# Kernel tuning notes

Measured on AMD Instinct MI355X. Metric: run time of the kernel, lower is better.

The kernel has to match this reference:

```python
import jax, jax.numpy as jnp
import numpy as np

B, NPG, D = 512, 200, 256  # graphs, nodes-per-graph, d_model
N = B * NPG
STEP = 4


def setup_inputs() -> dict:
    key = jax.random.key(0)
    ks = jax.random.split(key, 7)
    def xav(k, shape):
        fan_in, fan_out = shape[1], shape[0]
        std = float(np.sqrt(2.0 / (fan_in + fan_out)))
        return jax.random.normal(k, shape, jnp.float32) * std
    return {
        "node": jax.random.normal(ks[0], (N, D), jnp.float32),
        "node_num": jnp.full((B,), NPG, dtype=jnp.int32),
        "W_ih": xav(ks[1], (4 * D, 2 * D)),  # lstm weight_ih_l0
        "W_hh": xav(ks[2], (4 * D, D)),      # lstm weight_hh_l0
        "b_ih": jnp.zeros((4 * D,), jnp.float32),
        "b_hh": jnp.zeros((4 * D,), jnp.float32),
        "Wo": xav(ks[3], (D, 2 * D)),        # W_o.weight
        "bo": jnp.zeros((D,), jnp.float32),  # W_o.bias
    }


def reference(node, node_num, W_ih, W_hh, b_ih, b_hh, Wo, bo):
    n_total, d = node.shape
    bsz = node_num.shape[0]
    batch_idx = jnp.repeat(jnp.arange(bsz), node_num, total_repeat_length=n_total)
    h = jnp.zeros((bsz, d), node.dtype)
    c = jnp.zeros((bsz, d), node.dtype)
    q_star = jnp.zeros((bsz, 2 * d), node.dtype)
    for _ in range(STEP):
        # single-step LSTM (torch gate order: i, f, g, o)
        gates = q_star @ W_ih.T + h @ W_hh.T + b_ih + b_hh
        i, f, g, o = jnp.split(gates, 4, axis=-1)
        c = jax.nn.sigmoid(f) * c + jax.nn.sigmoid(i) * jnp.tanh(g)
        h = jax.nn.sigmoid(o) * jnp.tanh(c)
        q = h  # [B, d]
        # segmented softmax attention over nodes
        e = jnp.sum(node * q[batch_idx], axis=-1)  # [N]
        emax = jax.ops.segment_max(e, batch_idx, num_segments=bsz)
        e = jnp.exp(e - emax[batch_idx])
        denom = jax.ops.segment_sum(e, batch_idx, num_segments=bsz)
        a = e / (denom[batch_idx] + 1e-6)
        r = jax.ops.segment_sum(a[:, None] * node, batch_idx, num_segments=bsz)
        q_star = jnp.concatenate([q, r], axis=-1)
    return q_star @ Wo.T + bo
```

## Files before the change

kernel.cpp:

```cpp
#include <hip/hip_runtime.h>
#include <math.h>

#define DCH 256
#define BSZ 512
#define NPG 200
#define G4  1024
#define K2  512
#define KSD 4

typedef __attribute__((ext_vector_type(8))) short short8v;
typedef __attribute__((ext_vector_type(4))) float f32x4;

__device__ __forceinline__ float sigf(float x) { return 1.0f / (1.0f + __expf(-x)); }

__device__ __forceinline__ unsigned pack2bf(float a, float b) {
    unsigned ua = __float_as_uint(a), ub = __float_as_uint(b);
    ua = (ua + 0x7FFFu + ((ua >> 16) & 1u)) >> 16;
    ub = (ub + 0x7FFFu + ((ub >> 16) & 1u)) & 0xFFFF0000u;
    return ua | ub;
}
__device__ __forceinline__ float lo_bf(unsigned u) { return __uint_as_float(u << 16); }
__device__ __forceinline__ float hi_bf(unsigned u) { return __uint_as_float(u & 0xFFFF0000u); }

__global__ __launch_bounds__(256) void prep_kernel(
    const float* __restrict__ W_ih, const float* __restrict__ W_hh,
    const float* __restrict__ Wo,
    uint4* __restrict__ wcat, uint4* __restrict__ wobf)
{
    int idx = blockIdx.x * 256 + threadIdx.x;
    if (idx < 65536) {
        const int n = idx >> 6, k = (idx & 63) * 8;
        float v[8];
        *(float4*)(v)     = *(const float4*)(W_ih + (size_t)n * K2 + k);
        *(float4*)(v + 4) = *(const float4*)(W_ih + (size_t)n * K2 + k + 4);
        if (k < DCH) {
            float h[8];
            *(float4*)(h)     = *(const float4*)(W_hh + (size_t)n * DCH + k);
            *(float4*)(h + 4) = *(const float4*)(W_hh + (size_t)n * DCH + k + 4);
            #pragma unroll
            for (int i = 0; i < 8; ++i) v[i] += h[i];
        }
        uint4 u;
        u.x = pack2bf(v[0], v[1]); u.y = pack2bf(v[2], v[3]);
        u.z = pack2bf(v[4], v[5]); u.w = pack2bf(v[6], v[7]);
        wcat[idx] = u;
    } else {
        idx -= 65536;
        const int n = idx >> 6, k = (idx & 63) * 8;
        float v[8];
        *(float4*)(v)     = *(const float4*)(Wo + (size_t)n * K2 + k);
        *(float4*)(v + 4) = *(const float4*)(Wo + (size_t)n * K2 + k + 4);
        uint4 u;
        u.x = pack2bf(v[0], v[1]); u.y = pack2bf(v[2], v[3]);
        u.z = pack2bf(v[4], v[5]); u.w = pack2bf(v[6], v[7]);
        wobf[idx] = u;
    }
}

__global__ __launch_bounds__(256) void gemm_gates_mfma(
    const unsigned short* __restrict__ hrbf,
    const unsigned short* __restrict__ wcat,
    float* __restrict__ gpart, int Kper)
{
    const int wid  = threadIdx.x >> 6;
    const int lane = threadIdx.x & 63;
    const int bm = blockIdx.y * 64;
    const int bn = blockIdx.x * 128 + wid * 32;
    const int kbase = blockIdx.z * Kper;
    const int rsel = lane & 15, kgrp = lane >> 4;

    f32x4 acc00 = {}, acc01 = {}, acc10 = {}, acc11 = {},
          acc20 = {}, acc21 = {}, acc30 = {}, acc31 = {};

    for (int k0 = 0; k0 < Kper; k0 += 32) {
        const int kk = kbase + k0 + kgrp * 8;
        short8v a0 = *(const short8v*)(hrbf + (size_t)(bm +  0 + rsel) * K2 + kk);
        short8v a1 = *(const short8v*)(hrbf + (size_t)(bm + 16 + rsel) * K2 + kk);
        short8v a2 = *(const short8v*)(hrbf + (size_t)(bm + 32 + rsel) * K2 + kk);
        short8v a3 = *(const short8v*)(hrbf + (size_t)(bm + 48 + rsel) * K2 + kk);
        short8v b0 = *(const short8v*)(wcat + (size_t)(bn +  0 + rsel) * K2 + kk);
        short8v b1 = *(const short8v*)(wcat + (size_t)(bn + 16 + rsel) * K2 + kk);
        acc00 = __builtin_amdgcn_mfma_f32_16x16x32_bf16(a0, b0, acc00, 0, 0, 0);
        acc01 = __builtin_amdgcn_mfma_f32_16x16x32_bf16(a0, b1, acc01, 0, 0, 0);
        acc10 = __builtin_amdgcn_mfma_f32_16x16x32_bf16(a1, b0, acc10, 0, 0, 0);
        acc11 = __builtin_amdgcn_mfma_f32_16x16x32_bf16(a1, b1, acc11, 0, 0, 0);
        acc20 = __builtin_amdgcn_mfma_f32_16x16x32_bf16(a2, b0, acc20, 0, 0, 0);
        acc21 = __builtin_amdgcn_mfma_f32_16x16x32_bf16(a2, b1, acc21, 0, 0, 0);
        acc30 = __builtin_amdgcn_mfma_f32_16x16x32_bf16(a3, b0, acc30, 0, 0, 0);
        acc31 = __builtin_amdgcn_mfma_f32_16x16x32_bf16(a3, b1, acc31, 0, 0, 0);
    }

    float* Cp = gpart + (size_t)blockIdx.z * BSZ * G4;
    const int crow = kgrp * 4, ccol = rsel;
    const f32x4* accs[4][2] = { {&acc00, &acc01}, {&acc10, &acc11},
                                {&acc20, &acc21}, {&acc30, &acc31} };
    #pragma unroll
    for (int mi = 0; mi < 4; ++mi)
        #pragma unroll
        for (int ni = 0; ni < 2; ++ni)
            #pragma unroll
            for (int r = 0; r < 4; ++r)
                Cp[(size_t)(bm + mi * 16 + crow + r) * G4 + bn + ni * 16 + ccol] =
                    (*accs[mi][ni])[r];
}

template<int FIRST, int LAST>
__global__ __launch_bounds__(256) void lstm_attn_kernel(
    const float* __restrict__ gpart,
    const float* __restrict__ b_ih, const float* __restrict__ b_hh,
    const float* __restrict__ node, uint4* __restrict__ nbf,
    const int* __restrict__ node_num,
    float* __restrict__ cbuf, unsigned* __restrict__ hrbf,
    const uint4* __restrict__ wobf, const float* __restrict__ bo,
    float* __restrict__ outp)
{
    __shared__ __align__(16) float smem[4640];
    float* qs = smem;
    float (*red_r)[DCH] = (float (*)[DCH])(smem + 512);
    float* red_m = smem + 4608;
    float* red_s = smem + 4624;

    const int b = blockIdx.x;
    const int t = threadIdx.x;

    float gv[4];
    #pragma unroll
    for (int q = 0; q < 4; ++q) {
        const int idx = q * DCH + t;
        float v = b_ih[idx] + b_hh[idx];
        if (!FIRST) {
            #pragma unroll
            for (int z = 0; z < KSD; ++z)
                v += gpart[(size_t)z * BSZ * G4 + (size_t)b * G4 + idx];
        }
        gv[q] = v;
    }
    const float c_old = FIRST ? 0.0f : cbuf[b * DCH + t];
    const float cn = sigf(gv[1]) * c_old + sigf(gv[0]) * tanhf(gv[2]);
    const float hn = sigf(gv[3]) * tanhf(cn);
    if (!LAST) cbuf[b * DCH + t] = cn;
    qs[t] = hn;
    __syncthreads();

    const int w = t >> 6, l = t & 63;
    const int p = l & 15;
    const int g = w * 4 + (l >> 4);
    const int cnt = node_num[b];
    const float* nb = node + (size_t)b * NPG * DCH;
    uint4* nbf_b = nbf + (size_t)b * NPG * 32;

    float4 qv[4];
    #pragma unroll
    for (int j = 0; j < 2; ++j) {
        qv[j*2+0] = *(const float4*)(qs + j * 128 + p * 8);
        qv[j*2+1] = *(const float4*)(qs + j * 128 + p * 8 + 4);
    }

    auto ld_f32 = [&](int n, float4* x) {
        if (n < cnt) {
            #pragma unroll
            for (int j = 0; j < 2; ++j) {
                x[j*2+0] = *(const float4*)(nb + (size_t)n * DCH + j * 128 + p * 8);
                x[j*2+1] = *(const float4*)(nb + (size_t)n * DCH + j * 128 + p * 8 + 4);
            }
        } else {
            x[0] = x[1] = x[2] = x[3] = make_float4(0.f, 0.f, 0.f, 0.f);
        }
    };
    auto ld_bf = [&](int n, float4* x) {
        if (n < cnt) {
            #pragma unroll
            for (int j = 0; j < 2; ++j) {
                const uint4 u = nbf_b[(size_t)n * 32 + j * 16 + p];
                x[j*2+0] = make_float4(lo_bf(u.x), hi_bf(u.x), lo_bf(u.y), hi_bf(u.y));
                x[j*2+1] = make_float4(lo_bf(u.z), hi_bf(u.z), lo_bf(u.w), hi_bf(u.w));
            }
        } else {
            x[0] = x[1] = x[2] = x[3] = make_float4(0.f, 0.f, 0.f, 0.f);
        }
    };
    auto st_bf = [&](int n, const float4* x) {
        if (n < cnt) {
            #pragma unroll
            for (int j = 0; j < 2; ++j) {
                uint4 u;
                u.x = pack2bf(x[j*2+0].x, x[j*2+0].y);
                u.y = pack2bf(x[j*2+0].z, x[j*2+0].w);
                u.z = pack2bf(x[j*2+1].x, x[j*2+1].y);
                u.w = pack2bf(x[j*2+1].z, x[j*2+1].w);
                nbf_b[(size_t)n * 32 + j * 16 + p] = u;
            }
        }
    };

    float m = -INFINITY, s = 0.0f;
    float4 racc[4] = {};
    const int nit = (cnt + 31) >> 5;

    float4 x0[4], x1[4];
    if (FIRST) { ld_f32(2 * g, x0); ld_f32(2 * g + 1, x1); }
    else       { ld_bf (2 * g, x0); ld_bf (2 * g + 1, x1); }

    for (int it = 0; it < nit; ++it) {
        const int n0 = it * 32 + 2 * g;
        const int np = n0 + 32;
        float4 y0[4], y1[4];
        if (FIRST) { ld_f32(np, y0); ld_f32(np + 1, y1); }
        else       { ld_bf (np, y0); ld_bf (np + 1, y1); }
        if (FIRST) { st_bf(n0, x0); st_bf(n0 + 1, x1); }

        float e0 = 0.f, e1 = 0.f;
        #pragma unroll
        for (int j = 0; j < 4; ++j) {
            e0 += x0[j].x * qv[j].x + x0[j].y * qv[j].y + x0[j].z * qv[j].z + x0[j].w * qv[j].w;
            e1 += x1[j].x * qv[j].x + x1[j].y * qv[j].y + x1[j].z * qv[j].z + x1[j].w * qv[j].w;
        }
        #pragma unroll
        for (int off = 1; off < 16; off <<= 1) {
            e0 += __shfl_xor(e0, off);
            e1 += __shfl_xor(e1, off);
        }
        if (n0     >= cnt) e0 = -INFINITY;
        if (n0 + 1 >= cnt) e1 = -INFINITY;
        const float mn = fmaxf(m, fmaxf(e0, e1));
        if (mn > -INFINITY) {
            const float sc = __expf(m - mn);
            const float w0 = __expf(e0 - mn);
            const float w1 = __expf(e1 - mn);
            s = s * sc + w0 + w1;
            #pragma unroll
            for (int j = 0; j < 4; ++j) {
                racc[j].x = racc[j].x * sc + w0 * x0[j].x + w1 * x1[j].x;
                racc[j].y = racc[j].y * sc + w0 * x0[j].y + w1 * x1[j].y;
                racc[j].z = racc[j].z * sc + w0 * x0[j].z + w1 * x1[j].z;
                racc[j].w = racc[j].w * sc + w0 * x0[j].w + w1 * x1[j].w;
            }
            m = mn;
        }
        #pragma unroll
        for (int j = 0; j < 4; ++j) { x0[j] = y0[j]; x1[j] = y1[j]; }
    }

    #pragma unroll
    for (int j = 0; j < 2; ++j) {
        *(float4*)(&red_r[g][j * 128 + p * 8])     = racc[j*2+0];
        *(float4*)(&red_r[g][j * 128 + p * 8 + 4]) = racc[j*2+1];
    }
    if (p == 0) { red_m[g] = m; red_s[g] = s; }
    __syncthreads();

    float M = -INFINITY;
    #pragma unroll
    for (int g2 = 0; g2 < 16; ++g2) M = fmaxf(M, red_m[g2]);
    float stot = 0.0f, rtot = 0.0f;
    #pragma unroll
    for (int g2 = 0; g2 < 16; ++g2) {
        const float sc = __expf(red_m[g2] - M);
        stot += sc * red_s[g2];
        rtot += sc * red_r[g2][t];
    }
    rtot = rtot / (stot + 1e-6f);

    qs[256 + t] = rtot;
    __syncthreads();

    if (!LAST) {
        hrbf[b * 256 + t] = pack2bf(qs[2 * t], qs[2 * t + 1]);
        return;
    }

    float4 qv2[8];
    #pragma unroll
    for (int j = 0; j < 4; ++j) {
        qv2[j*2+0] = *(const float4*)(qs + j * 128 + p * 8);
        qv2[j*2+1] = *(const float4*)(qs + j * 128 + p * 8 + 4);
    }
    float* out_sm = smem + 512;

    #pragma unroll 2
    for (int v = 0; v < 8; ++v) {
        const int o0 = (2 * v) * 16 + g;
        const int o1 = o0 + 16;
        float e0 = 0.f, e1 = 0.f;
        #pragma unroll
        for (int j = 0; j < 4; ++j) {
            const uint4 ua = wobf[(size_t)o0 * 64 + j * 16 + p];
            const uint4 ub = wobf[(size_t)o1 * 64 + j * 16 + p];
            e0 += lo_bf(ua.x) * qv2[j*2].x + hi_bf(ua.x) * qv2[j*2].y
                + lo_bf(ua.y) * qv2[j*2].z + hi_bf(ua.y) * qv2[j*2].w
                + lo_bf(ua.z) * qv2[j*2+1].x + hi_bf(ua.z) * qv2[j*2+1].y
                + lo_bf(ua.w) * qv2[j*2+1].z + hi_bf(ua.w) * qv2[j*2+1].w;
            e1 += lo_bf(ub.x) * qv2[j*2].x + hi_bf(ub.x) * qv2[j*2].y
                + lo_bf(ub.y) * qv2[j*2].z + hi_bf(ub.y) * qv2[j*2].w
                + lo_bf(ub.z) * qv2[j*2+1].x + hi_bf(ub.z) * qv2[j*2+1].y
                + lo_bf(ub.w) * qv2[j*2+1].z + hi_bf(ub.w) * qv2[j*2+1].w;
        }
        #pragma unroll
        for (int off = 1; off < 16; off <<= 1) {
            e0 += __shfl_xor(e0, off);
            e1 += __shfl_xor(e1, off);
        }
        if (p == 0) {
            out_sm[o0] = e0 + bo[o0];
            out_sm[o1] = e1 + bo[o1];
        }
    }
    __syncthreads();
    outp[(size_t)b * DCH + t] = out_sm[t];
}

extern "C" void kernel_launch(void* const* d_in, const int* in_sizes, int n_in,
                              void* d_out, int out_size, void* d_ws, size_t ws_size,
                              hipStream_t stream)
{
    const float* node     = (const float*)d_in[0];
    const int*   node_num = (const int*)  d_in[1];
    const float* W_ih     = (const float*)d_in[2];
    const float* W_hh     = (const float*)d_in[3];
    const float* b_ih     = (const float*)d_in[4];
    const float* b_hh     = (const float*)d_in[5];
    const float* Wo       = (const float*)d_in[6];
    const float* bo       = (const float*)d_in[7];
    float* out = (float*)d_out;

    float* ws      = (float*)d_ws;
    float* cbuf    = ws;
    unsigned* hrbf = (unsigned*)(cbuf + BSZ * DCH);
    float* gpart   = (float*)(hrbf + BSZ * 256);
    uint4* wcat    = (uint4*)(gpart + (size_t)KSD * BSZ * G4);
    uint4* wobf    = wcat + 1024 * 64;
    uint4* nbf     = wobf + 256 * 64;

    prep_kernel<<<320, 256, 0, stream>>>(W_ih, W_hh, Wo, wcat, wobf);

    lstm_attn_kernel<1, 0><<<BSZ, 256, 0, stream>>>(
        gpart, b_ih, b_hh, node, nbf, node_num, cbuf, hrbf, wobf, bo, out);

    for (int s = 1; s < 4; ++s) {
        gemm_gates_mfma<<<dim3(8, 8, KSD), 256, 0, stream>>>(
            (const unsigned short*)hrbf, (const unsigned short*)wcat, gpart, K2 / KSD);
        if (s < 3) {
            lstm_attn_kernel<0, 0><<<BSZ, 256, 0, stream>>>(
                gpart, b_ih, b_hh, node, nbf, node_num, cbuf, hrbf, wobf, bo, out);
        } else {
            lstm_attn_kernel<0, 1><<<BSZ, 256, 0, stream>>>(
                gpart, b_ih, b_hh, node, nbf, node_num, cbuf, hrbf, wobf, bo, out);
        }
    }
}
```

Before: 102.7 us.

## Fuse weight prep into first attention kernel, deepen node prefetch, vectorize gate stores

```diff
diff --git a/kernel.cpp b/kernel.cpp
--- a/kernel.cpp
+++ b/kernel.cpp
@@ -22,41 +22,6 @@
 __device__ __forceinline__ float lo_bf(unsigned u) { return __uint_as_float(u << 16); }
 __device__ __forceinline__ float hi_bf(unsigned u) { return __uint_as_float(u & 0xFFFF0000u); }
 
-__global__ __launch_bounds__(256) void prep_kernel(
-    const float* __restrict__ W_ih, const float* __restrict__ W_hh,
-    const float* __restrict__ Wo,
-    uint4* __restrict__ wcat, uint4* __restrict__ wobf)
-{
-    int idx = blockIdx.x * 256 + threadIdx.x;
-    if (idx < 65536) {
-        const int n = idx >> 6, k = (idx & 63) * 8;
-        float v[8];
-        *(float4*)(v)     = *(const float4*)(W_ih + (size_t)n * K2 + k);
-        *(float4*)(v + 4) = *(const float4*)(W_ih + (size_t)n * K2 + k + 4);
-        if (k < DCH) {
-            float h[8];
-            *(float4*)(h)     = *(const float4*)(W_hh + (size_t)n * DCH + k);
-            *(float4*)(h + 4) = *(const float4*)(W_hh + (size_t)n * DCH + k + 4);
-            #pragma unroll
-            for (int i = 0; i < 8; ++i) v[i] += h[i];
-        }
-        uint4 u;
-        u.x = pack2bf(v[0], v[1]); u.y = pack2bf(v[2], v[3]);
-        u.z = pack2bf(v[4], v[5]); u.w = pack2bf(v[6], v[7]);
-        wcat[idx] = u;
-    } else {
-        idx -= 65536;
-        const int n = idx >> 6, k = (idx & 63) * 8;
-        float v[8];
-        *(float4*)(v)     = *(const float4*)(Wo + (size_t)n * K2 + k);
-        *(float4*)(v + 4) = *(const float4*)(Wo + (size_t)n * K2 + k + 4);
-        uint4 u;
-        u.x = pack2bf(v[0], v[1]); u.y = pack2bf(v[2], v[3]);
-        u.z = pack2bf(v[4], v[5]); u.w = pack2bf(v[6], v[7]);
-        wobf[idx] = u;
-    }
-}
-
 __global__ __launch_bounds__(256) void gemm_gates_mfma(
     const unsigned short* __restrict__ hrbf,
     const unsigned short* __restrict__ wcat,
@@ -64,44 +29,39 @@
 {
     const int wid  = threadIdx.x >> 6;
     const int lane = threadIdx.x & 63;
-    const int bm = blockIdx.y * 64;
-    const int bn = blockIdx.x * 128 + wid * 32;
+    const int gx = blockIdx.x * 128 + wid * 32;
+    const int gm = blockIdx.y * 64;
     const int kbase = blockIdx.z * Kper;
     const int rsel = lane & 15, kgrp = lane >> 4;
 
-    f32x4 acc00 = {}, acc01 = {}, acc10 = {}, acc11 = {},
-          acc20 = {}, acc21 = {}, acc30 = {}, acc31 = {};
+    f32x4 a0m0 = {}, a0m1 = {}, a0m2 = {}, a0m3 = {},
+          a1m0 = {}, a1m1 = {}, a1m2 = {}, a1m3 = {};
 
     for (int k0 = 0; k0 < Kper; k0 += 32) {
         const int kk = kbase + k0 + kgrp * 8;
-        short8v a0 = *(const short8v*)(hrbf + (size_t)(bm +  0 + rsel) * K2 + kk);
-        short8v a1 = *(const short8v*)(hrbf + (size_t)(bm + 16 + rsel) * K2 + kk);
-        short8v a2 = *(const short8v*)(hrbf + (size_t)(bm + 32 + rsel) * K2 + kk);
-        short8v a3 = *(const short8v*)(hrbf + (size_t)(bm + 48 + rsel) * K2 + kk);
-        short8v b0 = *(const short8v*)(wcat + (size_t)(bn +  0 + rsel) * K2 + kk);
-        short8v b1 = *(const short8v*)(wcat + (size_t)(bn + 16 + rsel) * K2 + kk);
-        acc00 = __builtin_amdgcn_mfma_f32_16x16x32_bf16(a0, b0, acc00, 0, 0, 0);
-        acc01 = __builtin_amdgcn_mfma_f32_16x16x32_bf16(a0, b1, acc01, 0, 0, 0);
-        acc10 = __builtin_amdgcn_mfma_f32_16x16x32_bf16(a1, b0, acc10, 0, 0, 0);
-        acc11 = __builtin_amdgcn_mfma_f32_16x16x32_bf16(a1, b1, acc11, 0, 0, 0);
-        acc20 = __builtin_amdgcn_mfma_f32_16x16x32_bf16(a2, b0, acc20, 0, 0, 0);
-        acc21 = __builtin_amdgcn_mfma_f32_16x16x32_bf16(a2, b1, acc21, 0, 0, 0);
-        acc30 = __builtin_amdgcn_mfma_f32_16x16x32_bf16(a3, b0, acc30, 0, 0, 0);
-        acc31 = __builtin_amdgcn_mfma_f32_16x16x32_bf16(a3, b1, acc31, 0, 0, 0);
+        short8v wa0 = *(const short8v*)(wcat + (size_t)(gx +  0 + rsel) * K2 + kk);
+        short8v wa1 = *(const short8v*)(wcat + (size_t)(gx + 16 + rsel) * K2 + kk);
+        short8v qb0 = *(const short8v*)(hrbf + (size_t)(gm +  0 + rsel) * K2 + kk);
+        short8v qb1 = *(const short8v*)(hrbf + (size_t)(gm + 16 + rsel) * K2 + kk);
+        short8v qb2 = *(const short8v*)(hrbf + (size_t)(gm + 32 + rsel) * K2 + kk);
+        short8v qb3 = *(const short8v*)(hrbf + (size_t)(gm + 48 + rsel) * K2 + kk);
+        a0m0 = __builtin_amdgcn_mfma_f32_16x16x32_bf16(wa0, qb0, a0m0, 0, 0, 0);
+        a0m1 = __builtin_amdgcn_mfma_f32_16x16x32_bf16(wa0, qb1, a0m1, 0, 0, 0);
+        a0m2 = __builtin_amdgcn_mfma_f32_16x16x32_bf16(wa0, qb2, a0m2, 0, 0, 0);
+        a0m3 = __builtin_amdgcn_mfma_f32_16x16x32_bf16(wa0, qb3, a0m3, 0, 0, 0);
+        a1m0 = __builtin_amdgcn_mfma_f32_16x16x32_bf16(wa1, qb0, a1m0, 0, 0, 0);
+        a1m1 = __builtin_amdgcn_mfma_f32_16x16x32_bf16(wa1, qb1, a1m1, 0, 0, 0);
+        a1m2 = __builtin_amdgcn_mfma_f32_16x16x32_bf16(wa1, qb2, a1m2, 0, 0, 0);
+        a1m3 = __builtin_amdgcn_mfma_f32_16x16x32_bf16(wa1, qb3, a1m3, 0, 0, 0);
     }
 
     float* Cp = gpart + (size_t)blockIdx.z * BSZ * G4;
-    const int crow = kgrp * 4, ccol = rsel;
-    const f32x4* accs[4][2] = { {&acc00, &acc01}, {&acc10, &acc11},
-                                {&acc20, &acc21}, {&acc30, &acc31} };
-    #pragma unroll
-    for (int mi = 0; mi < 4; ++mi)
-        #pragma unroll
-        for (int ni = 0; ni < 2; ++ni)
-            #pragma unroll
-            for (int r = 0; r < 4; ++r)
-                Cp[(size_t)(bm + mi * 16 + crow + r) * G4 + bn + ni * 16 + ccol] =
-                    (*accs[mi][ni])[r];
+    const int gr = kgrp * 4;
+    #define STORE_ACC(ni, mi, accv) \
+        *(f32x4*)(Cp + (size_t)(gm + (mi)*16 + rsel) * G4 + gx + (ni)*16 + gr) = (accv);
+    STORE_ACC(0, 0, a0m0) STORE_ACC(0, 1, a0m1) STORE_ACC(0, 2, a0m2) STORE_ACC(0, 3, a0m3)
+    STORE_ACC(1, 0, a1m0) STORE_ACC(1, 1, a1m1) STORE_ACC(1, 2, a1m2) STORE_ACC(1, 3, a1m3)
+    #undef STORE_ACC
 }
 
 template<int FIRST, int LAST>
@@ -111,8 +71,10 @@
     const float* __restrict__ node, uint4* __restrict__ nbf,
     const int* __restrict__ node_num,
     float* __restrict__ cbuf, unsigned* __restrict__ hrbf,
-    const uint4* __restrict__ wobf, const float* __restrict__ bo,
-    float* __restrict__ outp)
+    const float* __restrict__ W_ih, const float* __restrict__ W_hh,
+    const float* __restrict__ Wo,
+    uint4* __restrict__ wcat, uint4* __restrict__ wobf,
+    const float* __restrict__ bo, float* __restrict__ outp)
 {
     __shared__ __align__(16) float smem[4640];
     float* qs = smem;
@@ -122,6 +84,39 @@
 
     const int b = blockIdx.x;
     const int t = threadIdx.x;
+
+    if (FIRST) {
+        if (t < 160) {
+            int idx = blockIdx.x * 160 + t;
+            if (idx < 65536) {
+                const int n = idx >> 6, k = (idx & 63) * 8;
+                float v[8];
+                *(float4*)(v)     = *(const float4*)(W_ih + (size_t)n * K2 + k);
+                *(float4*)(v + 4) = *(const float4*)(W_ih + (size_t)n * K2 + k + 4);
+                if (k < DCH) {
+                    float h[8];
+                    *(float4*)(h)     = *(const float4*)(W_hh + (size_t)n * DCH + k);
+                    *(float4*)(h + 4) = *(const float4*)(W_hh + (size_t)n * DCH + k + 4);
+                    #pragma unroll
+                    for (int i = 0; i < 8; ++i) v[i] += h[i];
+                }
+                uint4 u;
+                u.x = pack2bf(v[0], v[1]); u.y = pack2bf(v[2], v[3]);
+                u.z = pack2bf(v[4], v[5]); u.w = pack2bf(v[6], v[7]);
+                wcat[idx] = u;
+            } else {
+                const int i2 = idx - 65536;
+                const int n = i2 >> 6, k = (i2 & 63) * 8;
+                float v[8];
+                *(float4*)(v)     = *(const float4*)(Wo + (size_t)n * K2 + k);
+                *(float4*)(v + 4) = *(const float4*)(Wo + (size_t)n * K2 + k + 4);
+                uint4 u;
+                u.x = pack2bf(v[0], v[1]); u.y = pack2bf(v[2], v[3]);
+                u.z = pack2bf(v[4], v[5]); u.w = pack2bf(v[6], v[7]);
+                wobf[i2] = u;
+            }
+        }
+    }
 
     float gv[4];
     #pragma unroll
@@ -156,24 +151,21 @@
         qv[j*2+1] = *(const float4*)(qs + j * 128 + p * 8 + 4);
     }
 
-    auto ld_f32 = [&](int n, float4* x) {
+    auto ld = [&](int n, float4* x) {
         if (n < cnt) {
-            #pragma unroll
-            for (int j = 0; j < 2; ++j) {
-                x[j*2+0] = *(const float4*)(nb + (size_t)n * DCH + j * 128 + p * 8);
-                x[j*2+1] = *(const float4*)(nb + (size_t)n * DCH + j * 128 + p * 8 + 4);
-            }
-        } else {
-            x[0] = x[1] = x[2] = x[3] = make_float4(0.f, 0.f, 0.f, 0.f);
-        }
-    };
-    auto ld_bf = [&](int n, float4* x) {
-        if (n < cnt) {
-            #pragma unroll
-            for (int j = 0; j < 2; ++j) {
-                const uint4 u = nbf_b[(size_t)n * 32 + j * 16 + p];
-                x[j*2+0] = make_float4(lo_bf(u.x), hi_bf(u.x), lo_bf(u.y), hi_bf(u.y));
-                x[j*2+1] = make_float4(lo_bf(u.z), hi_bf(u.z), lo_bf(u.w), hi_bf(u.w));
+            if (FIRST) {
+                #pragma unroll
+                for (int j = 0; j < 2; ++j) {
+                    x[j*2+0] = *(const float4*)(nb + (size_t)n * DCH + j * 128 + p * 8);
+                    x[j*2+1] = *(const float4*)(nb + (size_t)n * DCH + j * 128 + p * 8 + 4);
+                }
+            } else {
+                #pragma unroll
+                for (int j = 0; j < 2; ++j) {
+                    const uint4 u = nbf_b[(size_t)n * 32 + j * 16 + p];
+                    x[j*2+0] = make_float4(lo_bf(u.x), hi_bf(u.x), lo_bf(u.y), hi_bf(u.y));
+                    x[j*2+1] = make_float4(lo_bf(u.z), hi_bf(u.z), lo_bf(u.w), hi_bf(u.w));
+                }
             }
         } else {
             x[0] = x[1] = x[2] = x[3] = make_float4(0.f, 0.f, 0.f, 0.f);
@@ -197,16 +189,15 @@
     float4 racc[4] = {};
     const int nit = (cnt + 31) >> 5;
 
-    float4 x0[4], x1[4];
-    if (FIRST) { ld_f32(2 * g, x0); ld_f32(2 * g + 1, x1); }
-    else       { ld_bf (2 * g, x0); ld_bf (2 * g + 1, x1); }
+    float4 x0[4], x1[4], u0[4], u1[4];
+    ld(2 * g, x0);      ld(2 * g + 1, x1);
+    ld(32 + 2 * g, u0); ld(32 + 2 * g + 1, u1);
 
     for (int it = 0; it < nit; ++it) {
         const int n0 = it * 32 + 2 * g;
-        const int np = n0 + 32;
         float4 y0[4], y1[4];
-        if (FIRST) { ld_f32(np, y0); ld_f32(np + 1, y1); }
-        else       { ld_bf (np, y0); ld_bf (np + 1, y1); }
+        const int np = n0 + 64;
+        ld(np, y0); ld(np + 1, y1);
         if (FIRST) { st_bf(n0, x0); st_bf(n0 + 1, x1); }
 
         float e0 = 0.f, e1 = 0.f;
@@ -238,7 +229,10 @@
             m = mn;
         }
         #pragma unroll
-        for (int j = 0; j < 4; ++j) { x0[j] = y0[j]; x1[j] = y1[j]; }
+        for (int j = 0; j < 4; ++j) {
+            x0[j] = u0[j]; x1[j] = u1[j];
+            u0[j] = y0[j]; u1[j] = y1[j];
+        }
     }
 
     #pragma unroll
@@ -331,20 +325,21 @@
     uint4* wobf    = wcat + 1024 * 64;
     uint4* nbf     = wobf + 256 * 64;
 
-    prep_kernel<<<320, 256, 0, stream>>>(W_ih, W_hh, Wo, wcat, wobf);
-
     lstm_attn_kernel<1, 0><<<BSZ, 256, 0, stream>>>(
-        gpart, b_ih, b_hh, node, nbf, node_num, cbuf, hrbf, wobf, bo, out);
+        gpart, b_ih, b_hh, node, nbf, node_num, cbuf, hrbf,
+        W_ih, W_hh, Wo, wcat, wobf, bo, out);
 
     for (int s = 1; s < 4; ++s) {
         gemm_gates_mfma<<<dim3(8, 8, KSD), 256, 0, stream>>>(
             (const unsigned short*)hrbf, (const unsigned short*)wcat, gpart, K2 / KSD);
         if (s < 3) {
             lstm_attn_kernel<0, 0><<<BSZ, 256, 0, stream>>>(
-                gpart, b_ih, b_hh, node, nbf, node_num, cbuf, hrbf, wobf, bo, out);
+                gpart, b_ih, b_hh, node, nbf, node_num, cbuf, hrbf,
+                W_ih, W_hh, Wo, wcat, wobf, bo, out);
         } else {
             lstm_attn_kernel<0, 1><<<BSZ, 256, 0, stream>>>(
-                gpart, b_ih, b_hh, node, nbf, node_num, cbuf, hrbf, wobf, bo, out);
+                gpart, b_ih, b_hh, node, nbf, node_num, cbuf, hrbf,
+                W_ih, W_hh, Wo, wcat, wobf, bo, out);
         }
     }
 }
```

Result: faster. 100.5 us, median of 3 (-2.1%).
